# Performance work log

Measured on AMD Instinct MI355X. Metric: run time of the kernel, lower is better.

The kernel has to match this reference:

```python
import jax, jax.numpy as jnp
import numpy as np

B, S, D_EMBED, D_HIDDEN = 4, 256, 300, 300
C = 5.0  # frozen tanh-scaling constant


def setup_inputs() -> dict:
    key = jax.random.key(0)
    ks = jax.random.split(key, 8)
    w = 0.05  # ~xavier scale for 300x300
    return {
        "inputs": jax.random.normal(ks[0], (B, S, D_EMBED), jnp.float32),
        "rep_mask": jax.random.randint(ks[1], (B, S), 0, 2, jnp.int32),
        "W_fc": jax.random.normal(ks[2], (D_HIDDEN, D_EMBED), jnp.float32) * w,
        "b_fc": jnp.zeros((D_HIDDEN,), jnp.float32),
        "W1": jax.random.normal(ks[3], (D_HIDDEN, D_HIDDEN), jnp.float32) * w,
        "W2": jax.random.normal(ks[4], (D_HIDDEN, D_HIDDEN), jnp.float32) * w,
        "b1": jnp.zeros((D_HIDDEN,), jnp.float32),
        "W_f1": jax.random.normal(ks[5], (D_HIDDEN, D_HIDDEN), jnp.float32) * w,
        "W_f2": jax.random.normal(ks[6], (D_HIDDEN, D_HIDDEN), jnp.float32) * w,
        "b_f": jnp.zeros((D_HIDDEN,), jnp.float32),
    }


def _disa_fwd(inputs, rep_mask_f, W_fc, b_fc, W1, W2, b1, W_f1, W_f2, b_f):
    n_seq = inputs.shape[1]
    # forward direction mask: attend to strictly later positions (triu, diag=1)
    direct = jnp.triu(jnp.ones((n_seq, n_seq), inputs.dtype), k=1)
    # mask[b,i,j] = rep_mask[b,j] * direct[i,j], shape [B,S,S,1]
    mask = (rep_mask_f[:, None, :] * direct[None]) [..., None]

    rep_map = jax.nn.elu(jnp.einsum('bse,he->bsh', inputs, W_fc) + b_fc)  # [B,S,D]
    dep = jnp.einsum('bsh,gh->bsg', rep_map, W1)   # dependent (token j)
    head = jnp.einsum('bsh,gh->bsg', rep_map, W2)  # head (token i)

    # logits[b,i,j,d]
    logits = C * jnp.tanh((dep[:, None, :, :] + head[:, :, None, :] + b1) / C)

    # hand-rolled masked softmax over dim=2 (j), faithful to original
    masked = logits * mask
    mx = jnp.max(masked, axis=2, keepdims=True)
    exps = jnp.exp(masked - mx) * mask
    sums = jnp.sum(exps, axis=2, keepdims=True)
    sums = sums + (sums == 0).astype(logits.dtype)
    attn = (exps / (sums + 1e-20)) * mask

    attn_result = jnp.sum(attn * rep_map[:, None, :, :], axis=2)  # [B,S,D]

    gate = jax.nn.sigmoid(
        jnp.einsum('bsh,gh->bsg', rep_map, W_f1)
        + jnp.einsum('bsh,gh->bsg', attn_result, W_f2)
        + b_f
    )
    out = gate * rep_map + (1.0 - gate) * attn_result
    return out * rep_mask_f[..., None]


def reference(inputs, rep_mask, W_fc, b_fc, W1, W2, b1, W_f1, W_f2, b_f):
    rep_mask_f = rep_mask.astype(inputs.dtype)
    return _disa_fwd(inputs, rep_mask_f, W_fc, b_fc, W1, W2, b1, W_f1, W_f2, b_f)
```

## Files before the change

### kernel.cpp

```cpp
#include <hip/hip_runtime.h>
#include <hip/hip_bf16.h>

#define Dx 300

#define ED     0
#define HEADF  614400
#define ATTNF  921600
#define U_BASE 1228800
#define REPB   0
#define ATB    327680
#define SYNC_FOFF 2000000

#define AG __HIP_MEMORY_SCOPE_AGENT

typedef __attribute__((ext_vector_type(8))) short short8;
typedef __attribute__((ext_vector_type(4))) float f32x4;

union S8 { unsigned int u[4]; unsigned short s[8]; short8 v; };

__device__ __forceinline__ float bf2f(unsigned short u) {
    union { unsigned int i; float f; } v; v.i = ((unsigned int)u) << 16; return v.f;
}
__device__ __forceinline__ unsigned short f2bf(float x) {
    union { float f; unsigned int i; } u; u.f = x;
    return (unsigned short)((u.i + 0x8000u) >> 16);
}
__device__ __forceinline__ float ldf(const void* p, int idx, int isbf) {
    return isbf ? bf2f(((const unsigned short*)p)[idx]) : ((const float*)p)[idx];
}

__device__ __forceinline__ void st_wt_f32(float* p, float v) {
    asm volatile("global_store_dword %0, %1, off sc0 sc1"
                 :: "v"(p), "v"(v) : "memory");
}
__device__ __forceinline__ void st_wt_u16(unsigned short* p, unsigned short v) {
    unsigned int vv = v;
    asm volatile("global_store_short %0, %1, off sc0 sc1"
                 :: "v"(p), "v"(vv) : "memory");
}

__device__ __forceinline__ void load8f(const float* rowp, int kb, int kmax,
                                       int valid, float* x) {
    if (valid && kb + 8 <= kmax) {
        float4 a = *(const float4*)(rowp + kb);
        float4 b = *(const float4*)(rowp + kb + 4);
        x[0]=a.x; x[1]=a.y; x[2]=a.z; x[3]=a.w;
        x[4]=b.x; x[5]=b.y; x[6]=b.z; x[7]=b.w;
    } else {
        #pragma unroll
        for (int j = 0; j < 8; ++j) {
            int k = kb + j;
            x[j] = (valid && k < kmax) ? rowp[k] : 0.f;
        }
    }
}
__device__ __forceinline__ short8 pack8(const float* x) {
    S8 H;
    #pragma unroll
    for (int p = 0; p < 4; ++p) {
        union { float f; unsigned int i; } a, b;
        a.f = x[2*p]; b.f = x[2*p+1];
        H.u[p] = ((a.i + 0x8000u) >> 16) | ((b.i + 0x8000u) & 0xFFFF0000u);
    }
    return H.v;
}
__device__ __forceinline__ short8 load8bf(const unsigned short* rowp, int kb,
                                          int kmax, int valid) {
    S8 R;
    if (valid && kb + 8 <= kmax) {
        ushort4 a = *(const ushort4*)(rowp + kb);
        ushort4 b = *(const ushort4*)(rowp + kb + 4);
        R.s[0]=a.x; R.s[1]=a.y; R.s[2]=a.z; R.s[3]=a.w;
        R.s[4]=b.x; R.s[5]=b.y; R.s[6]=b.z; R.s[7]=b.w;
    } else {
        #pragma unroll
        for (int j = 0; j < 8; ++j) {
            int k = kb + j;
            R.s[j] = (valid && k < kmax) ? rowp[k] : (unsigned short)0;
        }
    }
    return R.v;
}
__device__ __forceinline__ short8 loadB(const void* W, int row, int kb, int isbf,
                                        int valid) {
    if (isbf) return load8bf((const unsigned short*)W + row * 300, kb, 300, valid);
    float t[8];
    load8f((const float*)W + row * 300, kb, 300, valid, t);
    return pack8(t);
}

__device__ __forceinline__ int xcd_id() {
    int x;
    asm volatile("s_getreg_b32 %0, hwreg(HW_REG_XCC_ID)" : "=s"(x));
    return x & 7;
}
__device__ __forceinline__ void spin_ge(int* p, int target) {
    int t = 0;
    while (__hip_atomic_load(p, __ATOMIC_RELAXED, AG) < target) {
        __builtin_amdgcn_s_sleep(1);
        if (++t > 500000) break;
    }
    asm volatile("" ::: "memory");
}


__global__ __launch_bounds__(320, 4) void k_fused(
        const void* __restrict__ Xv, const int* __restrict__ mask,
        const void* __restrict__ Wfc, const void* __restrict__ bfc,
        const void* __restrict__ W1,  const void* __restrict__ W2,
        const void* __restrict__ b1v, const void* __restrict__ Wf1,
        const void* __restrict__ Wf2, const void* __restrict__ bfv,
        float* __restrict__ ws, void* __restrict__ outv) {
    __shared__ int s_isbf;
    __shared__ unsigned short vlist[256];
    __shared__ int s_cnt, s_tgt;

    const int tid = threadIdx.x;
    const int blk = blockIdx.x;
    if (tid < 64) {
        float v = bf2f(((const unsigned short*)Wfc)[tid]);
        int ok = fabsf(v) < 1.0f;
        unsigned long long bal = __ballot(ok);
        if (tid == 0) s_isbf = (bal == ~0ull) ? 1 : 0;
    }
    __syncthreads();
    const int isbf = s_isbf;
    unsigned short* U = (unsigned short*)(ws + U_BASE);
    int* S = (int*)(ws + SYNC_FOFF);
    const int xid = xcd_id();

    const int res = blk & 7;
    const int bat = res >> 1;
    const int li  = ((blk >> 3) << 1) | (res & 1);
    const int base = bat * 256;

    if (li < 80 && tid < 256) {
        const int mt_l = li / 5, nt = li % 5;
        const int mt = bat * 16 + mt_l;
        const int w = tid >> 6, l = tid & 63;
        const int m0 = mt * 16, lm = l & 15, koff = (l >> 4) * 8;
        const int nrow = nt * 64 + w * 16 + lm;
        const int bval = nrow < 300;
        const int ncl = bval ? nrow : 0;
        f32x4 acc = {0.f, 0.f, 0.f, 0.f};
        if (isbf) {
            const unsigned short* Xp = (const unsigned short*)Xv + (m0 + lm) * 300;
            #pragma unroll
            for (int ks = 0; ks < 10; ++ks) {
                short8 a = load8bf(Xp, ks*32 + koff, 300, 1);
                short8 b = loadB(Wfc, ncl, ks*32 + koff, 1, bval);
                acc = __builtin_amdgcn_mfma_f32_16x16x32_bf16(a, b, acc, 0, 0, 0);
            }
        } else {
            const float* Xp = (const float*)Xv + (m0 + lm) * 300;
            #pragma unroll
            for (int ks = 0; ks < 10; ++ks) {
                float t[8]; load8f(Xp, ks*32 + koff, 300, 1, t);
                short8 a = pack8(t);
                short8 b = loadB(Wfc, ncl, ks*32 + koff, 0, bval);
                acc = __builtin_amdgcn_mfma_f32_16x16x32_bf16(a, b, acc, 0, 0, 0);
            }
        }
        if (bval) {
            float bb = ldf(bfc, nrow, isbf);
            #pragma unroll
            for (int r = 0; r < 4; ++r) {
                int mg = m0 + (l >> 4) * 4 + r;
                float v = acc[r] + bb;
                v = v > 0.f ? v : (__expf(v) - 1.f);
                st_wt_f32(ws + ED + (mg * 300 + nrow) * 2 + 1, v);
                st_wt_u16(U + REPB + mg * 320 + nrow, f2bf(v));
            }
        } else {
            #pragma unroll
            for (int r = 0; r < 4; ++r) {
                int mg = m0 + (l >> 4) * 4 + r;
                st_wt_u16(U + REPB + mg * 320 + nrow, 0);
            }
        }
    }
    __syncthreads();
    if (li < 80 && tid == 0)
        __hip_atomic_fetch_add(S + (bat * 16 + li / 5) * 64, 1,
                               __ATOMIC_RELAXED, AG);

    {
        const int mt_l = li / 10, nt10 = li % 10;
        const int mt = bat * 16 + mt_l;
        if (tid == 0) spin_ge(S + mt * 64, 5);
        __syncthreads();
        if (tid < 256) {
            const int w = tid >> 6, l = tid & 63;
            const int m0 = mt * 16, lm = l & 15, koff = (l >> 4) * 8;
            const int ng = nt10 * 64 + w * 16 + lm;
            const int wsel = ng < 320;
            const int wrow = wsel ? ng : ng - 320;
            const int bval = wrow < 300;
            const int ncl = bval ? wrow : 0;
            const void* Wsel = wsel ? W1 : W2;
            const unsigned short* ap = U + REPB + (m0 + lm) * 320 + koff;
            f32x4 acc = {0.f, 0.f, 0.f, 0.f};
            #pragma unroll
            for (int ks = 0; ks < 10; ++ks) {
                short8 a = *(const short8*)(ap + ks * 32);
                short8 b = loadB(Wsel, ncl, ks*32 + koff, isbf, bval);
                acc = __builtin_amdgcn_mfma_f32_16x16x32_bf16(a, b, acc, 0, 0, 0);
            }
            if (ng < 300) {
                float bb = ldf(b1v, ng, isbf);
                #pragma unroll
                for (int r = 0; r < 4; ++r) {
                    int mg = m0 + (l >> 4) * 4 + r;
                    st_wt_f32(ws + ED + (mg * 300 + ng) * 2,
                              __expf(0.4f * (acc[r] + bb)));
                }
            } else if (ng >= 320 && ng < 620) {
                #pragma unroll
                for (int r = 0; r < 4; ++r) {
                    int mg = m0 + (l >> 4) * 4 + r;
                    st_wt_f32(ws + HEADF + mg * 300 + (ng - 320), acc[r]);
                }
            }
        }
        __syncthreads();
        if (tid == 0) {
            int old = __hip_atomic_fetch_add(S + (64 + bat) * 64, 1,
                                             __ATOMIC_RELAXED, AG);
            if (old == 159) {
                #pragma unroll
                for (int x = 0; x < 8; ++x)
                    __hip_atomic_store(S + (68 + bat * 8 + x) * 64, 1,
                                       __ATOMIC_RELAXED, AG);
            }
        }
    }

    {
        if (tid < 64) {
            int basec = 0;
            #pragma unroll
            for (int c = 0; c < 4; ++c) {
                const int j = c * 64 + tid;
                const int mv = mask[base + j] != 0;
                unsigned long long bal = __ballot(mv);
                int pos = basec + __popcll(bal & ((1ull << tid) - 1ull));
                if (mv) vlist[pos] = (unsigned short)j;
                basec += __popcll(bal);
            }
            if (tid == 0) s_cnt = basec;
        }
        if (tid == 0) spin_ge(S + (68 + bat * 8 + xid) * 64, 1);
        __syncthreads();
        const int cnt = s_cnt;
        const int iu = 2 * li;
        if (iu < cnt) {
            const int ia = vlist[iu];
            const int hasB = (iu + 1 < cnt);
            const int ib = hasB ? vlist[iu + 1] : ia;
            const int ga = base + ia, gb = base + ib;
            const int d = tid;
            if (d >= 300) {
                st_wt_u16(U + ATB + ga * 320 + d, 0);
                if (hasB) st_wt_u16(U + ATB + gb * 320 + d, 0);
            } else {
                const float pwa = __expf(0.4f * ws[HEADF + ga * 300 + d]);
                const float pwb = __expf(0.4f * ws[HEADF + gb * 300 + d]);
                const float2* ep2 = ((const float2*)(ws + ED)) + base * Dx + d;
                float sa = 0.f, ra = 0.f, sb = 0.f, rb = 0.f;
                if (hasB) {
                    const int j = ib;
                    float2 v = ep2[j * Dx];
                    float ua = fmaf(v.x, pwa, 1.0f);
                    float ea = __expf(-10.0f * __builtin_amdgcn_rcpf(ua));
                    sa += ea; ra = fmaf(ea, v.y, ra);
                }
                #pragma unroll 16
                for (int t = iu + 2; t < cnt; ++t) {
                    const int j = vlist[t];
                    float2 v = ep2[j * Dx];
                    float ua = fmaf(v.x, pwa, 1.0f);
                    float ub = fmaf(v.x, pwb, 1.0f);
                    float ea = __expf(-10.0f * __builtin_amdgcn_rcpf(ua));
                    float eb = __expf(-10.0f * __builtin_amdgcn_rcpf(ub));
                    sa += ea; ra = fmaf(ea, v.y, ra);
                    sb += eb; rb = fmaf(eb, v.y, rb);
                }
                const float dena = sa + (sa == 0.f ? 1.f : 0.f) + 1e-20f;
                const float aa = ra / dena;
                st_wt_f32(ws + ATTNF + ga * Dx + d, aa);
                st_wt_u16(U + ATB + ga * 320 + d, f2bf(aa));
                if (hasB) {
                    const float denb = sb + (sb == 0.f ? 1.f : 0.f) + 1e-20f;
                    const float ab = rb / denb;
                    st_wt_f32(ws + ATTNF + gb * Dx + d, ab);
                    st_wt_u16(U + ATB + gb * 320 + d, f2bf(ab));
                }
            }
            __syncthreads();
            if (tid == 0) {
                __hip_atomic_fetch_add(S + (100 + (ga >> 4)) * 64, 1,
                                       __ATOMIC_RELAXED, AG);
                if (hasB)
                    __hip_atomic_fetch_add(S + (100 + (gb >> 4)) * 64, 1,
                                           __ATOMIC_RELAXED, AG);
            }
        }
    }

    if (li < 80) {
        const int mt3 = bat * 16 + li / 5, nt3 = li % 5;
        const int m0 = mt3 * 16;
        if (tid < 64) {
            int mv = (tid < 16) ? (mask[m0 + tid] != 0) : 0;
            unsigned long long bal = __ballot(mv);
            if (tid == 0) s_tgt = (int)__popcll(bal);
        }
        __syncthreads();
        const int tgt = s_tgt;
        if (tid == 0 && tgt > 0) spin_ge(S + (100 + mt3) * 64, tgt);
        __syncthreads();
        if (tid < 256) {
            const int w = tid >> 6, l = tid & 63;
            const int lm = l & 15, koff = (l >> 4) * 8;
            const int nrow = nt3 * 64 + w * 16 + lm;
            const int bval = nrow < 300;
            const int ncl = bval ? nrow : 0;
            const unsigned short* a1p = U + REPB + (m0 + lm) * 320 + koff;
            const unsigned short* a2p = U + ATB  + (m0 + lm) * 320 + koff;
            f32x4 acc = {0.f, 0.f, 0.f, 0.f};
            #pragma unroll
            for (int ks = 0; ks < 10; ++ks) {
                short8 a = *(const short8*)(a1p + ks * 32);
                short8 bB = loadB(Wf1, ncl, ks*32 + koff, isbf, bval);
                acc = __builtin_amdgcn_mfma_f32_16x16x32_bf16(a, bB, acc, 0, 0, 0);
            }
            #pragma unroll
            for (int ks = 0; ks < 10; ++ks) {
                short8 a = *(const short8*)(a2p + ks * 32);
                short8 bB = loadB(Wf2, ncl, ks*32 + koff, isbf, bval);
                acc = __builtin_amdgcn_mfma_f32_16x16x32_bf16(a, bB, acc, 0, 0, 0);
            }
            if (bval) {
                float bb = ldf(bfv, nrow, isbf);
                #pragma unroll
                for (int r = 0; r < 4; ++r) {
                    int mg = m0 + (l >> 4) * 4 + r;
                    float res2 = 0.f;
                    if (mask[mg]) {
                        float gp = acc[r] + bb;
                        float gate = 1.0f / (1.0f + __expf(-gp));
                        float rv = ws[ED + (mg * 300 + nrow) * 2 + 1];
                        float av = ws[ATTNF + mg * 300 + nrow];
                        res2 = gate * rv + (1.0f - gate) * av;
                    }
                    if (isbf) ((__hip_bfloat16*)outv)[mg * 300 + nrow] = __float2bfloat16(res2);
                    else      ((float*)outv)[mg * 300 + nrow] = res2;
                }
            }
        }
    }
}

extern "C" void kernel_launch(void* const* d_in, const int* in_sizes, int n_in,
                              void* d_out, int out_size, void* d_ws, size_t ws_size,
                              hipStream_t stream) {
    const void* X   = d_in[0];
    const int*  msk = (const int*)d_in[1];
    const void* Wfc = d_in[2];
    const void* bfc = d_in[3];
    const void* W1  = d_in[4];
    const void* W2  = d_in[5];
    const void* b1  = d_in[6];
    const void* Wf1 = d_in[7];
    const void* Wf2 = d_in[8];
    const void* bfv = d_in[9];
    float* ws = (float*)d_ws;

    hipMemsetAsync((char*)d_ws + (size_t)SYNC_FOFF * sizeof(float), 0, 49152, stream);

    hipLaunchKernelGGL(k_fused, dim3(640), dim3(320), 0, stream,
                       X, msk, Wfc, bfc, W1, W2, b1, Wf1, Wf2, bfv, ws, d_out);
}
```

Baseline: 114.2 us.

## Pin each batch to one XCD via atomic slot claiming and drop write-through stores

Blocks now read their hardware XCD id and claim a slot with an atomic counter, so each batch runs on one XCD (4 XCDs × 80 blocks) and surplus blocks exit early. Each surviving block handles two of the stage-2 and attention work units in a loop. The sc0 sc1 write-through stores become plain stores, relying on same-XCD L2 coherence, and the per-XCD ready flags collapse into one flag per batch. This aims to keep inter-block traffic inside one L2 and cut store latency, at the cost of using only half the XCDs and depending on the cache coherence assumption.

```diff
diff --git a/kernel.cpp b/kernel.cpp
--- a/kernel.cpp
+++ b/kernel.cpp
@@ -27,16 +27,6 @@
 }
 __device__ __forceinline__ float ldf(const void* p, int idx, int isbf) {
     return isbf ? bf2f(((const unsigned short*)p)[idx]) : ((const float*)p)[idx];
-}
-
-__device__ __forceinline__ void st_wt_f32(float* p, float v) {
-    asm volatile("global_store_dword %0, %1, off sc0 sc1"
-                 :: "v"(p), "v"(v) : "memory");
-}
-__device__ __forceinline__ void st_wt_u16(unsigned short* p, unsigned short v) {
-    unsigned int vv = v;
-    asm volatile("global_store_short %0, %1, off sc0 sc1"
-                 :: "v"(p), "v"(vv) : "memory");
 }
 
 __device__ __forceinline__ void load8f(const float* rowp, int kb, int kmax,
@@ -111,32 +101,38 @@
         const void* __restrict__ b1v, const void* __restrict__ Wf1,
         const void* __restrict__ Wf2, const void* __restrict__ bfv,
         float* __restrict__ ws, void* __restrict__ outv) {
-    __shared__ int s_isbf;
+    __shared__ int s_isbf, s_meta;
     __shared__ unsigned short vlist[256];
     __shared__ int s_cnt, s_tgt;
 
     const int tid = threadIdx.x;
-    const int blk = blockIdx.x;
-    if (tid < 64) {
-        float v = bf2f(((const unsigned short*)Wfc)[tid]);
+    int* S = (int*)(ws + SYNC_FOFF);
+
+    if (tid == 0) {
+        const int xid = xcd_id();
+        int slot = 1000;
+        if (xid < 4)
+            slot = __hip_atomic_fetch_add(S + (170 + xid) * 64, 1,
+                                          __ATOMIC_RELAXED, AG);
+        s_meta = (xid << 20) | (slot < 1000 ? slot : 1000);
+    }
+    if (tid >= 64 && tid < 128) {
+        float v = bf2f(((const unsigned short*)Wfc)[tid - 64]);
         int ok = fabsf(v) < 1.0f;
         unsigned long long bal = __ballot(ok);
-        if (tid == 0) s_isbf = (bal == ~0ull) ? 1 : 0;
+        if (tid == 64) s_isbf = (bal == ~0ull) ? 1 : 0;
     }
     __syncthreads();
+    const int meta = s_meta;
+    const int xid = meta >> 20, li = meta & 0xFFFFF;
+    if (xid >= 4 || li >= 80) return;
     const int isbf = s_isbf;
+    const int bat = xid;
+    const int base = bat * 256;
     unsigned short* U = (unsigned short*)(ws + U_BASE);
-    int* S = (int*)(ws + SYNC_FOFF);
-    const int xid = xcd_id();
-
-    const int res = blk & 7;
-    const int bat = res >> 1;
-    const int li  = ((blk >> 3) << 1) | (res & 1);
-    const int base = bat * 256;
-
-    if (li < 80 && tid < 256) {
-        const int mt_l = li / 5, nt = li % 5;
-        const int mt = bat * 16 + mt_l;
+
+    if (tid < 256) {
+        const int mt = bat * 16 + li / 5, nt = li % 5;
         const int w = tid >> 6, l = tid & 63;
         const int m0 = mt * 16, lm = l & 15, koff = (l >> 4) * 8;
         const int nrow = nt * 64 + w * 16 + lm;
@@ -168,25 +164,26 @@
                 int mg = m0 + (l >> 4) * 4 + r;
                 float v = acc[r] + bb;
                 v = v > 0.f ? v : (__expf(v) - 1.f);
-                st_wt_f32(ws + ED + (mg * 300 + nrow) * 2 + 1, v);
-                st_wt_u16(U + REPB + mg * 320 + nrow, f2bf(v));
+                ws[ED + (mg * 300 + nrow) * 2 + 1] = v;
+                U[REPB + mg * 320 + nrow] = f2bf(v);
             }
         } else {
             #pragma unroll
             for (int r = 0; r < 4; ++r) {
                 int mg = m0 + (l >> 4) * 4 + r;
-                st_wt_u16(U + REPB + mg * 320 + nrow, 0);
+                U[REPB + mg * 320 + nrow] = 0;
             }
         }
     }
     __syncthreads();
-    if (li < 80 && tid == 0)
+    if (tid == 0)
         __hip_atomic_fetch_add(S + (bat * 16 + li / 5) * 64, 1,
                                __ATOMIC_RELAXED, AG);
 
-    {
-        const int mt_l = li / 10, nt10 = li % 10;
-        const int mt = bat * 16 + mt_l;
+    #pragma unroll
+    for (int q = 0; q < 2; ++q) {
+        const int u = li + q * 80;
+        const int mt = bat * 16 + u / 10, nt10 = u % 10;
         if (tid == 0) spin_ge(S + mt * 64, 5);
         __syncthreads();
         if (tid < 256) {
@@ -211,14 +208,13 @@
                 #pragma unroll
                 for (int r = 0; r < 4; ++r) {
                     int mg = m0 + (l >> 4) * 4 + r;
-                    st_wt_f32(ws + ED + (mg * 300 + ng) * 2,
-                              __expf(0.4f * (acc[r] + bb)));
+                    ws[ED + (mg * 300 + ng) * 2] = __expf(0.4f * (acc[r] + bb));
                 }
             } else if (ng >= 320 && ng < 620) {
                 #pragma unroll
                 for (int r = 0; r < 4; ++r) {
                     int mg = m0 + (l >> 4) * 4 + r;
-                    st_wt_f32(ws + HEADF + mg * 300 + (ng - 320), acc[r]);
+                    ws[HEADF + mg * 300 + (ng - 320)] = acc[r];
                 }
             }
         }
@@ -226,12 +222,9 @@
         if (tid == 0) {
             int old = __hip_atomic_fetch_add(S + (64 + bat) * 64, 1,
                                              __ATOMIC_RELAXED, AG);
-            if (old == 159) {
-                #pragma unroll
-                for (int x = 0; x < 8; ++x)
-                    __hip_atomic_store(S + (68 + bat * 8 + x) * 64, 1,
-                                       __ATOMIC_RELAXED, AG);
-            }
+            if (old == 159)
+                __hip_atomic_store(S + (70 + bat) * 64, 1,
+                                   __ATOMIC_RELAXED, AG);
         }
     }
 
@@ -249,65 +242,67 @@
             }
             if (tid == 0) s_cnt = basec;
         }
-        if (tid == 0) spin_ge(S + (68 + bat * 8 + xid) * 64, 1);
+        if (tid == 0) spin_ge(S + (70 + bat) * 64, 1);
         __syncthreads();
         const int cnt = s_cnt;
-        const int iu = 2 * li;
-        if (iu < cnt) {
-            const int ia = vlist[iu];
-            const int hasB = (iu + 1 < cnt);
-            const int ib = hasB ? vlist[iu + 1] : ia;
-            const int ga = base + ia, gb = base + ib;
-            const int d = tid;
-            if (d >= 300) {
-                st_wt_u16(U + ATB + ga * 320 + d, 0);
-                if (hasB) st_wt_u16(U + ATB + gb * 320 + d, 0);
-            } else {
-                const float pwa = __expf(0.4f * ws[HEADF + ga * 300 + d]);
-                const float pwb = __expf(0.4f * ws[HEADF + gb * 300 + d]);
-                const float2* ep2 = ((const float2*)(ws + ED)) + base * Dx + d;
-                float sa = 0.f, ra = 0.f, sb = 0.f, rb = 0.f;
-                if (hasB) {
-                    const int j = ib;
-                    float2 v = ep2[j * Dx];
-                    float ua = fmaf(v.x, pwa, 1.0f);
-                    float ea = __expf(-10.0f * __builtin_amdgcn_rcpf(ua));
-                    sa += ea; ra = fmaf(ea, v.y, ra);
-                }
-                #pragma unroll 16
-                for (int t = iu + 2; t < cnt; ++t) {
-                    const int j = vlist[t];
-                    float2 v = ep2[j * Dx];
-                    float ua = fmaf(v.x, pwa, 1.0f);
-                    float ub = fmaf(v.x, pwb, 1.0f);
-                    float ea = __expf(-10.0f * __builtin_amdgcn_rcpf(ua));
-                    float eb = __expf(-10.0f * __builtin_amdgcn_rcpf(ub));
-                    sa += ea; ra = fmaf(ea, v.y, ra);
-                    sb += eb; rb = fmaf(eb, v.y, rb);
-                }
-                const float dena = sa + (sa == 0.f ? 1.f : 0.f) + 1e-20f;
-                const float aa = ra / dena;
-                st_wt_f32(ws + ATTNF + ga * Dx + d, aa);
-                st_wt_u16(U + ATB + ga * 320 + d, f2bf(aa));
-                if (hasB) {
-                    const float denb = sb + (sb == 0.f ? 1.f : 0.f) + 1e-20f;
-                    const float ab = rb / denb;
-                    st_wt_f32(ws + ATTNF + gb * Dx + d, ab);
-                    st_wt_u16(U + ATB + gb * 320 + d, f2bf(ab));
-                }
-            }
-            __syncthreads();
-            if (tid == 0) {
-                __hip_atomic_fetch_add(S + (100 + (ga >> 4)) * 64, 1,
-                                       __ATOMIC_RELAXED, AG);
-                if (hasB)
-                    __hip_atomic_fetch_add(S + (100 + (gb >> 4)) * 64, 1,
+        #pragma unroll
+        for (int q = 0; q < 2; ++q) {
+            const int iu = 2 * (li + q * 80);
+            if (iu < cnt) {
+                const int ia = vlist[iu];
+                const int hasB = (iu + 1 < cnt);
+                const int ib = hasB ? vlist[iu + 1] : ia;
+                const int ga = base + ia, gb = base + ib;
+                const int d = tid;
+                if (d >= 300) {
+                    U[ATB + ga * 320 + d] = 0;
+                    if (hasB) U[ATB + gb * 320 + d] = 0;
+                } else {
+                    const float pwa = __expf(0.4f * ws[HEADF + ga * 300 + d]);
+                    const float pwb = __expf(0.4f * ws[HEADF + gb * 300 + d]);
+                    const float2* ep2 = ((const float2*)(ws + ED)) + base * Dx + d;
+                    float sa = 0.f, ra = 0.f, sb = 0.f, rb = 0.f;
+                    if (hasB) {
+                        float2 v = ep2[ib * Dx];
+                        float ua = fmaf(v.x, pwa, 1.0f);
+                        float ea = __expf(-10.0f * __builtin_amdgcn_rcpf(ua));
+                        sa += ea; ra = fmaf(ea, v.y, ra);
+                    }
+                    #pragma unroll 8
+                    for (int t = iu + 2; t < cnt; ++t) {
+                        const int j = vlist[t];
+                        float2 v = ep2[j * Dx];
+                        float ua = fmaf(v.x, pwa, 1.0f);
+                        float ub = fmaf(v.x, pwb, 1.0f);
+                        float ea = __expf(-10.0f * __builtin_amdgcn_rcpf(ua));
+                        float eb = __expf(-10.0f * __builtin_amdgcn_rcpf(ub));
+                        sa += ea; ra = fmaf(ea, v.y, ra);
+                        sb += eb; rb = fmaf(eb, v.y, rb);
+                    }
+                    const float dena = sa + (sa == 0.f ? 1.f : 0.f) + 1e-20f;
+                    const float aa = ra / dena;
+                    ws[ATTNF + ga * Dx + d] = aa;
+                    U[ATB + ga * 320 + d] = f2bf(aa);
+                    if (hasB) {
+                        const float denb = sb + (sb == 0.f ? 1.f : 0.f) + 1e-20f;
+                        const float ab = rb / denb;
+                        ws[ATTNF + gb * Dx + d] = ab;
+                        U[ATB + gb * 320 + d] = f2bf(ab);
+                    }
+                }
+                __syncthreads();
+                if (tid == 0) {
+                    __hip_atomic_fetch_add(S + (100 + (ga >> 4)) * 64, 1,
                                            __ATOMIC_RELAXED, AG);
-            }
-        }
-    }
-
-    if (li < 80) {
+                    if (hasB)
+                        __hip_atomic_fetch_add(S + (100 + (gb >> 4)) * 64, 1,
+                                               __ATOMIC_RELAXED, AG);
+                }
+            }
+        }
+    }
+
+    {
         const int mt3 = bat * 16 + li / 5, nt3 = li % 5;
         const int m0 = mt3 * 16;
         if (tid < 64) {
@@ -378,6 +373,6 @@
 
     hipMemsetAsync((char*)d_ws + (size_t)SYNC_FOFF * sizeof(float), 0, 49152, stream);
 
-    hipLaunchKernelGGL(k_fused, dim3(640), dim3(320), 0, stream,
+    hipLaunchKernelGGL(k_fused, dim3(1024), dim3(320), 0, stream,
                        X, msk, Wfc, bfc, W1, W2, b1, Wf1, Wf2, bfv, ws, d_out);
 }
```

Result: slower. 137.1 us (+20.0%).

## Split fused persistent kernel into two launches, replacing per-batch spin barrier

Applied to the files above, without the earlier changes.

The single persistent kernel is split in two. The first kernel computes the FC+ELU projection and the dep/head projections. The second runs the masked attention and the gate GEMM, so the kernel boundary replaces the batch-wide atomic counter and spin-wait that sat between those phases. Write-through stores become plain stores, the attention loop unroll drops from 16 to 8, and block counts and sizes change per kernel. This trades spin-wait and occupancy limits for an extra launch, while phase one still relies on intra-kernel spins for its row-tile dependency.

```diff
diff --git a/kernel.cpp b/kernel.cpp
--- a/kernel.cpp
+++ b/kernel.cpp
@@ -89,54 +89,42 @@
     return pack8(t);
 }
 
-__device__ __forceinline__ int xcd_id() {
-    int x;
-    asm volatile("s_getreg_b32 %0, hwreg(HW_REG_XCC_ID)" : "=s"(x));
-    return x & 7;
-}
+__device__ __forceinline__ int detect_isbf(const void* Wfc, int tid, int* s_isbf) {
+    if (tid < 64) {
+        float v = bf2f(((const unsigned short*)Wfc)[tid]);
+        int ok = fabsf(v) < 1.0f;
+        unsigned long long bal = __ballot(ok);
+        if (tid == 0) *s_isbf = (bal == ~0ull) ? 1 : 0;
+    }
+    __syncthreads();
+    return *s_isbf;
+}
+
 __device__ __forceinline__ void spin_ge(int* p, int target) {
     int t = 0;
     while (__hip_atomic_load(p, __ATOMIC_RELAXED, AG) < target) {
         __builtin_amdgcn_s_sleep(1);
-        if (++t > 500000) break;
+        if (++t > 400000) break;
     }
     asm volatile("" ::: "memory");
 }
 
 
-__global__ __launch_bounds__(320, 4) void k_fused(
-        const void* __restrict__ Xv, const int* __restrict__ mask,
-        const void* __restrict__ Wfc, const void* __restrict__ bfc,
-        const void* __restrict__ W1,  const void* __restrict__ W2,
-        const void* __restrict__ b1v, const void* __restrict__ Wf1,
-        const void* __restrict__ Wf2, const void* __restrict__ bfv,
-        float* __restrict__ ws, void* __restrict__ outv) {
+__global__ __launch_bounds__(256) void k_a(
+        const void* __restrict__ Xv, const void* __restrict__ Wfc,
+        const void* __restrict__ bfc, const void* __restrict__ W1,
+        const void* __restrict__ W2,  const void* __restrict__ b1v,
+        float* __restrict__ ws) {
     __shared__ int s_isbf;
-    __shared__ unsigned short vlist[256];
-    __shared__ int s_cnt, s_tgt;
-
-    const int tid = threadIdx.x;
-    const int blk = blockIdx.x;
-    if (tid < 64) {
-        float v = bf2f(((const unsigned short*)Wfc)[tid]);
-        int ok = fabsf(v) < 1.0f;
-        unsigned long long bal = __ballot(ok);
-        if (tid == 0) s_isbf = (bal == ~0ull) ? 1 : 0;
-    }
-    __syncthreads();
-    const int isbf = s_isbf;
+    const int tid = threadIdx.x, blk = blockIdx.x;
+    const int isbf = detect_isbf(Wfc, tid, &s_isbf);
     unsigned short* U = (unsigned short*)(ws + U_BASE);
     int* S = (int*)(ws + SYNC_FOFF);
-    const int xid = xcd_id();
-
-    const int res = blk & 7;
-    const int bat = res >> 1;
-    const int li  = ((blk >> 3) << 1) | (res & 1);
-    const int base = bat * 256;
-
-    if (li < 80 && tid < 256) {
-        const int mt_l = li / 5, nt = li % 5;
-        const int mt = bat * 16 + mt_l;
+    const int bat = (blk & 7) >> 1;
+    const int li  = ((blk >> 3) << 1) | (blk & 1);
+
+    if (li < 80) {
+        const int mt = bat * 16 + li / 5, nt = li % 5;
         const int w = tid >> 6, l = tid & 63;
         const int m0 = mt * 16, lm = l & 15, koff = (l >> 4) * 8;
         const int nrow = nt * 64 + w * 16 + lm;
@@ -168,7 +156,7 @@
                 int mg = m0 + (l >> 4) * 4 + r;
                 float v = acc[r] + bb;
                 v = v > 0.f ? v : (__expf(v) - 1.f);
-                st_wt_f32(ws + ED + (mg * 300 + nrow) * 2 + 1, v);
+                ws[ED + (mg * 300 + nrow) * 2 + 1] = v;
                 st_wt_u16(U + REPB + mg * 320 + nrow, f2bf(v));
             }
         } else {
@@ -185,55 +173,57 @@
                                __ATOMIC_RELAXED, AG);
 
     {
-        const int mt_l = li / 10, nt10 = li % 10;
-        const int mt = bat * 16 + mt_l;
+        const int mt = bat * 16 + li / 10, nt10 = li % 10;
         if (tid == 0) spin_ge(S + mt * 64, 5);
         __syncthreads();
-        if (tid < 256) {
-            const int w = tid >> 6, l = tid & 63;
-            const int m0 = mt * 16, lm = l & 15, koff = (l >> 4) * 8;
-            const int ng = nt10 * 64 + w * 16 + lm;
-            const int wsel = ng < 320;
-            const int wrow = wsel ? ng : ng - 320;
-            const int bval = wrow < 300;
-            const int ncl = bval ? wrow : 0;
-            const void* Wsel = wsel ? W1 : W2;
-            const unsigned short* ap = U + REPB + (m0 + lm) * 320 + koff;
-            f32x4 acc = {0.f, 0.f, 0.f, 0.f};
-            #pragma unroll
-            for (int ks = 0; ks < 10; ++ks) {
-                short8 a = *(const short8*)(ap + ks * 32);
-                short8 b = loadB(Wsel, ncl, ks*32 + koff, isbf, bval);
-                acc = __builtin_amdgcn_mfma_f32_16x16x32_bf16(a, b, acc, 0, 0, 0);
-            }
-            if (ng < 300) {
-                float bb = ldf(b1v, ng, isbf);
-                #pragma unroll
-                for (int r = 0; r < 4; ++r) {
-                    int mg = m0 + (l >> 4) * 4 + r;
-                    st_wt_f32(ws + ED + (mg * 300 + ng) * 2,
-                              __expf(0.4f * (acc[r] + bb)));
-                }
-            } else if (ng >= 320 && ng < 620) {
-                #pragma unroll
-                for (int r = 0; r < 4; ++r) {
-                    int mg = m0 + (l >> 4) * 4 + r;
-                    st_wt_f32(ws + HEADF + mg * 300 + (ng - 320), acc[r]);
-                }
-            }
-        }
-        __syncthreads();
-        if (tid == 0) {
-            int old = __hip_atomic_fetch_add(S + (64 + bat) * 64, 1,
-                                             __ATOMIC_RELAXED, AG);
-            if (old == 159) {
-                #pragma unroll
-                for (int x = 0; x < 8; ++x)
-                    __hip_atomic_store(S + (68 + bat * 8 + x) * 64, 1,
-                                       __ATOMIC_RELAXED, AG);
-            }
-        }
-    }
+        const int w = tid >> 6, l = tid & 63;
+        const int m0 = mt * 16, lm = l & 15, koff = (l >> 4) * 8;
+        const int ng = nt10 * 64 + w * 16 + lm;
+        const int wsel = ng < 320;
+        const int wrow = wsel ? ng : ng - 320;
+        const int bval = wrow < 300;
+        const int ncl = bval ? wrow : 0;
+        const void* Wsel = wsel ? W1 : W2;
+        const unsigned short* ap = U + REPB + (m0 + lm) * 320 + koff;
+        f32x4 acc = {0.f, 0.f, 0.f, 0.f};
+        #pragma unroll
+        for (int ks = 0; ks < 10; ++ks) {
+            short8 a = *(const short8*)(ap + ks * 32);
+            short8 b = loadB(Wsel, ncl, ks*32 + koff, isbf, bval);
+            acc = __builtin_amdgcn_mfma_f32_16x16x32_bf16(a, b, acc, 0, 0, 0);
+        }
+        if (ng < 300) {
+            float bb = ldf(b1v, ng, isbf);
+            #pragma unroll
+            for (int r = 0; r < 4; ++r) {
+                int mg = m0 + (l >> 4) * 4 + r;
+                ws[ED + (mg * 300 + ng) * 2] = __expf(0.4f * (acc[r] + bb));
+            }
+        } else if (ng >= 320 && ng < 620) {
+            #pragma unroll
+            for (int r = 0; r < 4; ++r) {
+                int mg = m0 + (l >> 4) * 4 + r;
+                ws[HEADF + mg * 300 + (ng - 320)] = acc[r];
+            }
+        }
+    }
+}
+
+__global__ __launch_bounds__(320) void k_b(
+        const void* __restrict__ Wfc, const void* __restrict__ Wf1,
+        const void* __restrict__ Wf2, const void* __restrict__ bfv,
+        const int* __restrict__ mask, float* __restrict__ ws,
+        void* __restrict__ outv) {
+    __shared__ int s_isbf;
+    __shared__ unsigned short vlist[256];
+    __shared__ int s_cnt, s_tgt;
+    const int tid = threadIdx.x, blk = blockIdx.x;
+    const int isbf = detect_isbf(Wfc, tid, &s_isbf);
+    unsigned short* U = (unsigned short*)(ws + U_BASE);
+    int* S = (int*)(ws + SYNC_FOFF);
+    const int bat = (blk & 7) >> 1;
+    const int li  = ((blk >> 3) << 1) | (blk & 1);
+    const int base = bat * 256;
 
     {
         if (tid < 64) {
@@ -249,7 +239,6 @@
             }
             if (tid == 0) s_cnt = basec;
         }
-        if (tid == 0) spin_ge(S + (68 + bat * 8 + xid) * 64, 1);
         __syncthreads();
         const int cnt = s_cnt;
         const int iu = 2 * li;
@@ -268,13 +257,12 @@
                 const float2* ep2 = ((const float2*)(ws + ED)) + base * Dx + d;
                 float sa = 0.f, ra = 0.f, sb = 0.f, rb = 0.f;
                 if (hasB) {
-                    const int j = ib;
-                    float2 v = ep2[j * Dx];
+                    float2 v = ep2[ib * Dx];
                     float ua = fmaf(v.x, pwa, 1.0f);
                     float ea = __expf(-10.0f * __builtin_amdgcn_rcpf(ua));
                     sa += ea; ra = fmaf(ea, v.y, ra);
                 }
-                #pragma unroll 16
+                #pragma unroll 8
                 for (int t = iu + 2; t < cnt; ++t) {
                     const int j = vlist[t];
                     float2 v = ep2[j * Dx];
@@ -304,6 +292,8 @@
                     __hip_atomic_fetch_add(S + (100 + (gb >> 4)) * 64, 1,
                                            __ATOMIC_RELAXED, AG);
             }
+        } else {
+            __syncthreads();
         }
     }
 
@@ -345,16 +335,16 @@
                 #pragma unroll
                 for (int r = 0; r < 4; ++r) {
                     int mg = m0 + (l >> 4) * 4 + r;
-                    float res2 = 0.f;
+                    float res = 0.f;
                     if (mask[mg]) {
                         float gp = acc[r] + bb;
                         float gate = 1.0f / (1.0f + __expf(-gp));
                         float rv = ws[ED + (mg * 300 + nrow) * 2 + 1];
                         float av = ws[ATTNF + mg * 300 + nrow];
-                        res2 = gate * rv + (1.0f - gate) * av;
+                        res = gate * rv + (1.0f - gate) * av;
                     }
-                    if (isbf) ((__hip_bfloat16*)outv)[mg * 300 + nrow] = __float2bfloat16(res2);
-                    else      ((float*)outv)[mg * 300 + nrow] = res2;
+                    if (isbf) ((__hip_bfloat16*)outv)[mg * 300 + nrow] = __float2bfloat16(res);
+                    else      ((float*)outv)[mg * 300 + nrow] = res;
                 }
             }
         }
@@ -378,6 +368,8 @@
 
     hipMemsetAsync((char*)d_ws + (size_t)SYNC_FOFF * sizeof(float), 0, 49152, stream);
 
-    hipLaunchKernelGGL(k_fused, dim3(640), dim3(320), 0, stream,
-                       X, msk, Wfc, bfc, W1, W2, b1, Wf1, Wf2, bfv, ws, d_out);
-}
+    hipLaunchKernelGGL(k_a, dim3(640), dim3(256), 0, stream,
+                       X, Wfc, bfc, W1, W2, b1, ws);
+    hipLaunchKernelGGL(k_b, dim3(512), dim3(320), 0, stream,
+                       Wfc, Wf1, Wf2, bfv, msk, ws, d_out);
+}
```

New measurement: 118.5 us. 3.8% more time.
